# Kernel tuning notes

Measured on AMD Instinct MI355X. Metric: run time of the kernel, lower is better.

## Reference

```python
import jax, jax.numpy as jnp
import numpy as np

WBIT = 8
ABIT = 8
NESTBIT = 4
SHIFTBIT = WBIT - NESTBIT  # 4
OUT, IN, TOKENS = 8192, 8192, 256


def setup_inputs() -> dict:
    key = jax.random.key(0)
    ks = jax.random.split(key, 6)
    x = jax.random.normal(ks[0], (TOKENS, IN), dtype=jnp.float32)
    # two 4-bit high-group values packed per byte along in_features
    packed_high = jax.random.randint(ks[1], (OUT, IN // 2), 0, 256, dtype=jnp.int32)
    # 5-bit low-group values (offset-16 signed), one per byte
    packed_low = jax.random.randint(ks[2], (OUT, IN), 0, 32, dtype=jnp.int32)
    scale = jax.random.uniform(ks[3], (OUT, 1), dtype=jnp.float32) * 0.01 + 1e-4
    zero_point = jax.random.normal(ks[4], (OUT, 1), dtype=jnp.float32)
    bias = jax.random.normal(ks[5], (OUT,), dtype=jnp.float32)
    act_scale = jnp.ones((), dtype=jnp.float32) * 0.05
    return {"x": x, "packed_high": packed_high, "packed_low": packed_low,
            "scale": scale, "zero_point": zero_point, "bias": bias,
            "act_scale": act_scale}


def _quant_input(x, s):
    # abit symmetric fake-quant with straight-through estimator
    n = 2 ** (ABIT - 1)
    xq = jnp.clip(jnp.round(x / s), -n, n - 1) * s
    return x + jax.lax.stop_gradient(xq - x)


def _dequant_weight(packed_high, packed_low, scale, zero_point):
    # unpack two 4-bit nibbles per byte -> signed [-8, 7]
    hi = (packed_high >> 4) & 0xF
    lo = packed_high & 0xF
    qh = jnp.stack([hi, lo], axis=-1).reshape(packed_high.shape[0], -1) - 8  # [OUT, IN]
    ql = packed_low - 16  # 5-bit signed [-16, 15]
    n = 2 ** (WBIT - 1)
    q = jnp.clip(qh * (2 ** SHIFTBIT) + ql, -n, n - 1)
    # linear_dequantize; torch wraps this in no_grad -> weight is a constant
    w = (q.astype(jnp.float32) - zero_point) * scale
    return jax.lax.stop_gradient(w)


def reference(x, packed_high, packed_low, scale, zero_point, bias, act_scale):
    xq = _quant_input(x, act_scale)
    w = _dequant_weight(packed_high, packed_low, scale, zero_point)  # [OUT, IN]
    return jnp.dot(xq, w.T) + bias  # [TOKENS, OUT]
```

## Files before the change

### kernel.cpp

```cpp
#include <hip/hip_runtime.h>


typedef int v4i __attribute__((ext_vector_type(4)));

#define TOKENS 256
#define INF 8192
#define OUTF 8192
#define NSTEP 32

__global__ __launch_bounds__(256) void quant_x_kernel(
    const float* __restrict__ x, const float* __restrict__ act_scale,
    int* __restrict__ apk, int* __restrict__ rowsum)
{
    const int t = blockIdx.x;
    const int j = threadIdx.x;
    const float s = act_scale[0];
    const float4* xrow = (const float4*)(x + (size_t)t * INF);
    const int f    = t >> 4;
    const int llow = t & 15;
    int lsum = 0;
#pragma unroll
    for (int c = 0; c < 8; ++c) {
        const int kw = j + c * 256;
        float4 v = xrow[kw];
        int q0 = (int)rintf(v.x / s); q0 = q0 < -128 ? -128 : (q0 > 127 ? 127 : q0);
        int q1 = (int)rintf(v.y / s); q1 = q1 < -128 ? -128 : (q1 > 127 ? 127 : q1);
        int q2 = (int)rintf(v.z / s); q2 = q2 < -128 ? -128 : (q2 > 127 ? 127 : q2);
        int q3 = (int)rintf(v.w / s); q3 = q3 < -128 ? -128 : (q3 > 127 ? 127 : q3);
        const int word = (q0 & 255) | ((q1 & 255) << 8) | ((q2 & 255) << 16) | ((q3 & 255) << 24);
        const int k0 = kw << 2;
        const int kb = k0 >> 6;
        const int ks = k0 & 63;
        const int lane = ((ks >> 4) << 4) + llow;
        apk[kb * 4096 + f * 256 + (lane << 2) + ((ks & 15) >> 2)] = word;
        lsum += q0 + q1 + q2 + q3;
    }
#pragma unroll
    for (int off = 32; off > 0; off >>= 1) lsum += __shfl_down(lsum, off, 64);
    __shared__ int wsum[4];
    if ((j & 63) == 0) wsum[j >> 6] = lsum;
    __syncthreads();
    if (j == 0) rowsum[t] = wsum[0] + wsum[1] + wsum[2] + wsum[3];
}

__device__ __forceinline__ int unpack4(v4i pl, int pha, int phb) {
    int q0 = (pha & 0xF0)        + pl[0] - 144; q0 = q0 < -128 ? -128 : q0;
    int q1 = ((pha & 0x0F) << 4) + pl[1] - 144; q1 = q1 < -128 ? -128 : q1;
    int q2 = (phb & 0xF0)        + pl[2] - 144; q2 = q2 < -128 ? -128 : q2;
    int q3 = ((phb & 0x0F) << 4) + pl[3] - 144; q3 = q3 < -128 ? -128 : q3;
    return (q0 & 255) | ((q1 & 255) << 8) | ((q2 & 255) << 16) | ((q3 & 255) << 24);
}

__global__ __launch_bounds__(256) void gemm_kernel(
    const int* __restrict__ apk, const int* __restrict__ rowsum,
    const int* __restrict__ packed_high, const int* __restrict__ packed_low,
    const float* __restrict__ scale, const float* __restrict__ zero_point,
    const float* __restrict__ bias, const float* __restrict__ act_scale,
    float* __restrict__ out)
{
    __shared__ int accbuf[16][4][64];

    const int tid  = threadIdx.x;
    const int lane = tid & 63;
    const int w    = tid >> 6;
    const int n0   = blockIdx.x * 16;
    const int col  = lane & 15;
    const int kq16 = lane >> 4;

    const int o     = n0 + col;
    const int kbase = w * (NSTEP * 64) + kq16 * 16;
    const int* pl = packed_low  + (size_t)o * INF       + kbase;
    const int* ph = packed_high + (size_t)o * (INF / 2) + (kbase >> 1);

    const int* ab = apk + w * NSTEP * 4096 + (lane << 2);

    v4i acc[16];
#pragma unroll
    for (int f = 0; f < 16; ++f) acc[f] = (v4i){0, 0, 0, 0};

    v4i a[16], plv[4], phv[2];
#pragma unroll
    for (int m = 0; m < 4; ++m) plv[m] = *(const v4i*)(pl + 4 * m);
#pragma unroll
    for (int m = 0; m < 2; ++m) phv[m] = *(const v4i*)(ph + 4 * m);
#pragma unroll
    for (int f = 0; f < 16; ++f) a[f] = *(const v4i*)(ab + f * 256);

    for (int t = 0; t < NSTEP; ++t) {
        const int tn = (t + 1) & (NSTEP - 1);
        v4i b;
        b[0] = unpack4(plv[0], phv[0][0], phv[0][1]);
        b[1] = unpack4(plv[1], phv[0][2], phv[0][3]);
        b[2] = unpack4(plv[2], phv[1][0], phv[1][1]);
        b[3] = unpack4(plv[3], phv[1][2], phv[1][3]);
#pragma unroll
        for (int m = 0; m < 4; ++m) plv[m] = *(const v4i*)(pl + tn * 64 + 4 * m);
#pragma unroll
        for (int m = 0; m < 2; ++m) phv[m] = *(const v4i*)(ph + tn * 32 + 4 * m);
        const int* abn = ab + tn * 4096;
#pragma unroll
        for (int f = 0; f < 16; ++f) {
            acc[f] = __builtin_amdgcn_mfma_i32_16x16x64_i8(a[f], b, acc[f], 0, 0, 0);
            a[f] = *(const v4i*)(abn + f * 256);
        }
    }

    int* flat = &accbuf[0][0][0];
#pragma unroll
    for (int i = 0; i < 4; ++i) *(v4i*)(flat + tid * 16 + i * 4) = (v4i){0, 0, 0, 0};
    __syncthreads();
#pragma unroll
    for (int f = 0; f < 16; ++f)
#pragma unroll
        for (int r = 0; r < 4; ++r)
            atomicAdd(&accbuf[f][r][lane], acc[f][r]);
    __syncthreads();

    const float as = act_scale[0];
    const float sc = as * scale[o];
    const float zo = zero_point[o];
    const float bo = bias[o];
#pragma unroll
    for (int ff = 0; ff < 4; ++ff) {
        const int f = (w << 2) + ff;
        const int rbase = f * 16 + kq16 * 4;
        v4i rs = *(const v4i*)(rowsum + rbase);
#pragma unroll
        for (int r = 0; r < 4; ++r) {
            const float fv = (float)accbuf[f][r][lane] - zo * (float)rs[r];
            out[(size_t)(rbase + r) * OUTF + o] = fmaf(sc, fv, bo);
        }
    }
}

extern "C" void kernel_launch(void* const* d_in, const int* in_sizes, int n_in,
                              void* d_out, int out_size, void* d_ws, size_t ws_size,
                              hipStream_t stream)
{
    const float* x           = (const float*)d_in[0];
    const int*   packed_high = (const int*)d_in[1];
    const int*   packed_low  = (const int*)d_in[2];
    const float* scale       = (const float*)d_in[3];
    const float* zero_point  = (const float*)d_in[4];
    const float* bias        = (const float*)d_in[5];
    const float* act_scale   = (const float*)d_in[6];
    float* out = (float*)d_out;

    int* apk    = (int*)d_ws;
    int* rowsum = (int*)((char*)d_ws + (size_t)TOKENS * INF);

    quant_x_kernel<<<TOKENS, 256, 0, stream>>>(x, act_scale, apk, rowsum);
    gemm_kernel<<<OUTF / 16, 256, 0, stream>>>(apk, rowsum, packed_high, packed_low,
                                               scale, zero_point, bias, act_scale, out);
}
```

Measured before the change: 492.8 us.

## Share unpacked weights via LDS and split tokens across blocks instead of K

The GEMM switches from per-wave K-splitting (16 token-frags per wave, reduced through LDS atomics) to having each wave unpack a K slice of weights into a double-buffered LDS tile that all four waves read, with each wave computing 32 tokens over full K. The grid doubles so each block handles half the tokens, and occupancy hints are added. This removes the LDS atomic reduction and the large register footprint, but the packed weights are now read and unpacked twice (once per token half), and there is a barrier every step.

```diff
diff --git a/kernel.cpp b/kernel.cpp
--- a/kernel.cpp
+++ b/kernel.cpp
@@ -6,7 +6,8 @@
 #define TOKENS 256
 #define INF 8192
 #define OUTF 8192
-#define NSTEP 32
+#define KSTEP 256
+#define NITER 32
 
 __global__ __launch_bounds__(256) void quant_x_kernel(
     const float* __restrict__ x, const float* __restrict__ act_scale,
@@ -51,85 +52,98 @@
     return (q0 & 255) | ((q1 & 255) << 8) | ((q2 & 255) << 16) | ((q3 & 255) << 24);
 }
 
-__global__ __launch_bounds__(256) void gemm_kernel(
+__global__ __launch_bounds__(256, 4) void gemm_kernel(
     const int* __restrict__ apk, const int* __restrict__ rowsum,
     const int* __restrict__ packed_high, const int* __restrict__ packed_low,
     const float* __restrict__ scale, const float* __restrict__ zero_point,
     const float* __restrict__ bias, const float* __restrict__ act_scale,
     float* __restrict__ out)
 {
-    __shared__ int accbuf[16][4][64];
+    __shared__ __align__(16) signed char Bu[2][4096];
 
     const int tid  = threadIdx.x;
     const int lane = tid & 63;
     const int w    = tid >> 6;
-    const int n0   = blockIdx.x * 16;
-    const int col  = lane & 15;
-    const int kq16 = lane >> 4;
+    const int bid  = blockIdx.x;
+    const int H    = bid >> 9;
+    const int n0   = (bid & 511) << 4;
+    const int c    = lane & 15;
+    const int kq   = lane >> 4;
+    const int o    = n0 + c;
 
-    const int o     = n0 + col;
-    const int kbase = w * (NSTEP * 64) + kq16 * 16;
-    const int* pl = packed_low  + (size_t)o * INF       + kbase;
-    const int* ph = packed_high + (size_t)o * (INF / 2) + (kbase >> 1);
+    const int ksh = (w << 6) + (kq << 4);
+    const int* pl_p = packed_low  + (size_t)o * INF       + ksh;
+    const int* ph_p = packed_high + (size_t)o * (INF / 2) + (ksh >> 1);
+    const int wof = ((w << 2) + kq) * 256 + (c << 4);
+    const int rof = (kq << 8) + (c << 4);
 
-    const int* ab = apk + w * NSTEP * 4096 + (lane << 2);
+    const int* a_p = apk + (((H << 3) + (w << 1)) << 8) + (lane << 2);
 
-    v4i acc[16];
-#pragma unroll
-    for (int f = 0; f < 16; ++f) acc[f] = (v4i){0, 0, 0, 0};
+    v4i acc0 = {0,0,0,0}, acc1 = {0,0,0,0};
+    v4i plP[4], phP[2], plQ[4], phQ[2];
 
-    v4i a[16], plv[4], phv[2];
-#pragma unroll
-    for (int m = 0; m < 4; ++m) plv[m] = *(const v4i*)(pl + 4 * m);
-#pragma unroll
-    for (int m = 0; m < 2; ++m) phv[m] = *(const v4i*)(ph + 4 * m);
-#pragma unroll
-    for (int f = 0; f < 16; ++f) a[f] = *(const v4i*)(ab + f * 256);
+#define LOADPK(PL, PH, T) {                                                     \
+        const int kk_ = ((T) & (NITER - 1)) * KSTEP;                            \
+        _Pragma("unroll")                                                       \
+        for (int m = 0; m < 4; ++m) PL[m] = *(const v4i*)(pl_p + kk_ + 4 * m);  \
+        _Pragma("unroll")                                                       \
+        for (int m = 0; m < 2; ++m) PH[m] = *(const v4i*)(ph_p + (kk_ >> 1) + 4 * m); }
 
-    for (int t = 0; t < NSTEP; ++t) {
-        const int tn = (t + 1) & (NSTEP - 1);
-        v4i b;
-        b[0] = unpack4(plv[0], phv[0][0], phv[0][1]);
-        b[1] = unpack4(plv[1], phv[0][2], phv[0][3]);
-        b[2] = unpack4(plv[2], phv[1][0], phv[1][1]);
-        b[3] = unpack4(plv[3], phv[1][2], phv[1][3]);
-#pragma unroll
-        for (int m = 0; m < 4; ++m) plv[m] = *(const v4i*)(pl + tn * 64 + 4 * m);
-#pragma unroll
-        for (int m = 0; m < 2; ++m) phv[m] = *(const v4i*)(ph + tn * 32 + 4 * m);
-        const int* abn = ab + tn * 4096;
-#pragma unroll
-        for (int f = 0; f < 16; ++f) {
-            acc[f] = __builtin_amdgcn_mfma_i32_16x16x64_i8(a[f], b, acc[f], 0, 0, 0);
-            a[f] = *(const v4i*)(abn + f * 256);
-        }
+#define HALF(PL, PH, BUF, T) {                                                        \
+        v4i u;                                                                        \
+        u[0] = unpack4(PL[0], PH[0][0], PH[0][1]);                                    \
+        u[1] = unpack4(PL[1], PH[0][2], PH[0][3]);                                    \
+        u[2] = unpack4(PL[2], PH[1][0], PH[1][1]);                                    \
+        u[3] = unpack4(PL[3], PH[1][2], PH[1][3]);                                    \
+        *(v4i*)(&Bu[BUF][wof]) = u;                                                   \
+                                    \
+        const int kb_ = (T) << 2;                                                     \
+        v4i a0 = *(const v4i*)(a_p + (kb_ + 0) * 4096);                               \
+        v4i a1 = *(const v4i*)(a_p + (kb_ + 0) * 4096 + 256);                         \
+        v4i a2 = *(const v4i*)(a_p + (kb_ + 1) * 4096);                               \
+        v4i a3 = *(const v4i*)(a_p + (kb_ + 1) * 4096 + 256);                         \
+        v4i a4 = *(const v4i*)(a_p + (kb_ + 2) * 4096);                               \
+        v4i a5 = *(const v4i*)(a_p + (kb_ + 2) * 4096 + 256);                         \
+        v4i a6 = *(const v4i*)(a_p + (kb_ + 3) * 4096);                               \
+        v4i a7 = *(const v4i*)(a_p + (kb_ + 3) * 4096 + 256);                         \
+               \
+        LOADPK(PL, PH, (T) + 2);                                                      \
+        asm volatile("" ::: "memory");          \
+        asm volatile("s_waitcnt lgkmcnt(0)" ::: "memory");      \
+        __builtin_amdgcn_s_barrier();                                                 \
+        v4i b0 = *(const v4i*)(&Bu[BUF][rof]);                                        \
+        v4i b1 = *(const v4i*)(&Bu[BUF][1024 + rof]);                                 \
+        v4i b2 = *(const v4i*)(&Bu[BUF][2048 + rof]);                                 \
+        v4i b3 = *(const v4i*)(&Bu[BUF][3072 + rof]);                                 \
+        acc0 = __builtin_amdgcn_mfma_i32_16x16x64_i8(a0, b0, acc0, 0, 0, 0);          \
+        acc1 = __builtin_amdgcn_mfma_i32_16x16x64_i8(a1, b0, acc1, 0, 0, 0);          \
+        acc0 = __builtin_amdgcn_mfma_i32_16x16x64_i8(a2, b1, acc0, 0, 0, 0);          \
+        acc1 = __builtin_amdgcn_mfma_i32_16x16x64_i8(a3, b1, acc1, 0, 0, 0);          \
+        acc0 = __builtin_amdgcn_mfma_i32_16x16x64_i8(a4, b2, acc0, 0, 0, 0);          \
+        acc1 = __builtin_amdgcn_mfma_i32_16x16x64_i8(a5, b2, acc1, 0, 0, 0);          \
+        acc0 = __builtin_amdgcn_mfma_i32_16x16x64_i8(a6, b3, acc0, 0, 0, 0);          \
+        acc1 = __builtin_amdgcn_mfma_i32_16x16x64_i8(a7, b3, acc1, 0, 0, 0); }
+
+    LOADPK(plP, phP, 0);
+    LOADPK(plQ, phQ, 1);
+    for (int t = 0; t < NITER; t += 2) {
+        HALF(plP, phP, 0, t);
+        HALF(plQ, phQ, 1, t + 1);
     }
-
-    int* flat = &accbuf[0][0][0];
-#pragma unroll
-    for (int i = 0; i < 4; ++i) *(v4i*)(flat + tid * 16 + i * 4) = (v4i){0, 0, 0, 0};
-    __syncthreads();
-#pragma unroll
-    for (int f = 0; f < 16; ++f)
-#pragma unroll
-        for (int r = 0; r < 4; ++r)
-            atomicAdd(&accbuf[f][r][lane], acc[f][r]);
-    __syncthreads();
+#undef HALF
+#undef LOADPK
 
     const float as = act_scale[0];
     const float sc = as * scale[o];
     const float zo = zero_point[o];
     const float bo = bias[o];
+    const int f0 = (H << 3) + (w << 1);
 #pragma unroll
-    for (int ff = 0; ff < 4; ++ff) {
-        const int f = (w << 2) + ff;
-        const int rbase = f * 16 + kq16 * 4;
-        v4i rs = *(const v4i*)(rowsum + rbase);
-#pragma unroll
-        for (int r = 0; r < 4; ++r) {
-            const float fv = (float)accbuf[f][r][lane] - zo * (float)rs[r];
-            out[(size_t)(rbase + r) * OUTF + o] = fmaf(sc, fv, bo);
-        }
+    for (int r = 0; r < 4; ++r) {
+        const int t0 = f0 * 16 + (kq << 2) + r;
+        const int t1 = t0 + 16;
+        out[(size_t)t0 * OUTF + o] = fmaf(sc, (float)acc0[r] - zo * (float)rowsum[t0], bo);
+        out[(size_t)t1 * OUTF + o] = fmaf(sc, (float)acc1[r] - zo * (float)rowsum[t1], bo);
     }
 }
 
@@ -150,6 +164,6 @@
     int* rowsum = (int*)((char*)d_ws + (size_t)TOKENS * INF);
 
     quant_x_kernel<<<TOKENS, 256, 0, stream>>>(x, act_scale, apk, rowsum);
-    gemm_kernel<<<OUTF / 16, 256, 0, stream>>>(apk, rowsum, packed_high, packed_low,
-                                               scale, zero_point, bias, act_scale, out);
+    gemm_kernel<<<1024, 256, 0, stream>>>(apk, rowsum, packed_high, packed_low,
+                                          scale, zero_point, bias, act_scale, out);
 }
```

Measured after the change: 546.0 us. +10.8%, slower.
